# Kernel tuning notes

Hardware: AMD Instinct MI355X
Metric: run time of the kernel (lower is better)

The kernel has to match this reference:

```python
import jax, jax.numpy as jnp
import numpy as np

D_MODEL = 1024
N_HEADS = 16
D_HEAD = D_MODEL // N_HEADS


def setup_inputs() -> dict:
    key = jax.random.key(0)
    ks = jax.random.split(key, 11)
    B, S = 2, 2048
    scale = 1.0 / np.sqrt(D_MODEL)
    inp = {
        "query": jax.random.normal(ks[0], (B, S, D_MODEL), jnp.float32),
        "key": jax.random.normal(ks[1], (B, S, D_MODEL), jnp.float32),
        "value": jax.random.normal(ks[2], (B, S, D_MODEL), jnp.float32),
        "Wq": jax.random.normal(ks[3], (D_MODEL, D_MODEL), jnp.float32) * scale,
        "bq": jnp.zeros((D_MODEL,), jnp.float32),
        "Wk": jax.random.normal(ks[4], (D_MODEL, D_MODEL), jnp.float32) * scale,
        "bk": jnp.zeros((D_MODEL,), jnp.float32),
        "Wv": jax.random.normal(ks[5], (D_MODEL, D_MODEL), jnp.float32) * scale,
        "bv": jnp.zeros((D_MODEL,), jnp.float32),
        "Wo": jax.random.normal(ks[6], (D_MODEL, D_MODEL), jnp.float32) * scale,
        "bo": jnp.zeros((D_MODEL,), jnp.float32),
    }
    return inp


def _split_heads(x):
    B, S, _ = x.shape
    return x.reshape(B, S, N_HEADS, D_HEAD).transpose(0, 2, 1, 3)  # [B,H,S,Dh]


def reference(query, key, value, Wq, bq, Wk, bk, Wv, bv, Wo, bo):
    q = _split_heads(query @ Wq + bq)
    k = _split_heads(key @ Wk + bk)
    v = _split_heads(value @ Wv + bv)
    # scores [B,H,S,S] -- faithfully materialized as in the original
    scores = jnp.einsum("bhqd,bhkd->bhqk", q, k) / np.sqrt(D_HEAD)
    attn = jax.nn.softmax(scores, axis=-1)
    out = jnp.einsum("bhqk,bhkd->bhqd", attn, v)  # [B,H,S,Dh]
    B, H, S, Dh = out.shape
    out = out.transpose(0, 2, 1, 3).reshape(B, S, H * Dh)
    return out @ Wo + bo
```

## Files before the change

### kernel.cpp

```cpp
#include <hip/hip_runtime.h>
#include <hip/hip_bf16.h>

using bf16 = __hip_bfloat16;
typedef __bf16 bf16x8 __attribute__((ext_vector_type(8)));
typedef __bf16 bf16x2v __attribute__((ext_vector_type(2)));
typedef float f32x4 __attribute__((ext_vector_type(4)));
typedef float f32x16 __attribute__((ext_vector_type(16)));

#define SEQ 2048
#define DM  1024
#define QSCALE 0.18033688011112042f

__device__ __forceinline__ f32x4 mfma16(bf16x8 a, bf16x8 b, f32x4 c) {
  return __builtin_amdgcn_mfma_f32_16x16x32_bf16(a, b, c, 0, 0, 0);
}
__device__ __forceinline__ f32x16 mfma32(bf16x8 a, bf16x8 b, f32x16 c) {
  return __builtin_amdgcn_mfma_f32_32x32x16_bf16(a, b, c, 0, 0, 0);
}
__device__ __forceinline__ void gload16(const void* g, void* l) {
  __builtin_amdgcn_global_load_lds(
      (const __attribute__((address_space(1))) unsigned int*)g,
      (__attribute__((address_space(3))) unsigned int*)l, 16, 0, 0);
}
__device__ __forceinline__ unsigned short bfbits(float x) {
  bf16 h = __float2bfloat16(x);
  return *reinterpret_cast<unsigned short*>(&h);
}
__device__ __forceinline__ unsigned pk2(float a, float b) {
#if __has_builtin(__builtin_amdgcn_cvt_pk_bf16_f32)
  bf16x2v r = __builtin_amdgcn_cvt_pk_bf16_f32(a, b);
  return *reinterpret_cast<unsigned*>(&r);
#else
  return (unsigned)bfbits(a) | ((unsigned)bfbits(b) << 16);
#endif
}
__device__ __forceinline__ float fexp2(float x) {
#if __has_builtin(__builtin_amdgcn_exp2f)
  return __builtin_amdgcn_exp2f(x);
#else
  return exp2f(x);
#endif
}
__device__ __forceinline__ void plswap(unsigned& a, unsigned& b) {
  asm("v_permlane32_swap_b32 %0, %1" : "+v"(a), "+v"(b));
}

__global__ __launch_bounds__(256) void cast_all(const float* __restrict__ q,
                                                const float* __restrict__ k,
                                                const float* __restrict__ v,
                                                const float* __restrict__ Wq,
                                                const float* __restrict__ Wk,
                                                const float* __restrict__ Wv,
                                                const float* __restrict__ Wo,
                                                bf16* __restrict__ Lx,
                                                bf16* __restrict__ Lw,
                                                bf16* __restrict__ Lwo) {
  __shared__ float tf[64][68];
  if (blockIdx.y < 3) {
    const float* src = blockIdx.y == 0 ? q : (blockIdx.y == 1 ? k : v);
    bf16* dst = Lx + (size_t)blockIdx.y * (4096ull * 1024) + (size_t)blockIdx.x * 16384;
#pragma unroll
    for (int i = 0; i < 8; ++i) {
      int u = threadIdx.x + i * 256;
      int k32 = u >> 6, l = u & 63;
      const float* p = src + (size_t)(blockIdx.x * 16 + (l & 15)) * 1024 + k32 * 32 + (l >> 4) * 8;
      float4 a = *(const float4*)p;
      float4 b = *(const float4*)(p + 4);
      alignas(16) unsigned o[4] = {pk2(a.x, a.y), pk2(a.z, a.w), pk2(b.x, b.y), pk2(b.z, b.w)};
      *(uint4*)(dst + (size_t)u * 8) = *(const uint4*)o;
    }
    return;
  }
  const int widx = blockIdx.y - 3;
  const float* W = widx == 0 ? Wq : (widx == 1 ? Wk : (widx == 2 ? Wv : Wo));
  bf16* dst = widx < 3 ? (Lw + (size_t)widx * 1048576) : Lwo;
  const int t = threadIdx.x, bx = blockIdx.x & 15, by = blockIdx.x >> 4;
#pragma unroll
  for (int i = 0; i < 4; ++i) {
    int u = t + i * 256, r = u >> 4, c4 = u & 15;
    *(float4*)&tf[r][c4 * 4] = *(const float4*)(W + (size_t)(by * 64 + r) * 1024 + bx * 64 + c4 * 4);
  }
  __syncthreads();
#pragma unroll
  for (int i = 0; i < 2; ++i) {
    int u = t + i * 256;
    int sub = u >> 6, l = u & 63;
    int n16l = sub >> 1, k32l = sub & 1;
    int nn = n16l * 16 + (l & 15);
    int kk = k32l * 32 + (l >> 4) * 8;
    alignas(16) unsigned o[4];
#pragma unroll
    for (int p = 0; p < 4; ++p) o[p] = pk2(tf[kk + 2 * p][nn], tf[kk + 2 * p + 1][nn]);
    size_t off = ((((size_t)(bx * 4 + n16l)) * 32 + (by * 2 + k32l)) * 64 + l) * 8;
    *(uint4*)(dst + off) = *(const uint4*)o;
  }
}

__global__ __launch_bounds__(256) void qkv_gemm(const bf16* __restrict__ Lw,
                                                const bf16* __restrict__ Lx,
                                                const float* __restrict__ bq,
                                                const float* __restrict__ bk,
                                                const float* __restrict__ bv,
                                                bf16* __restrict__ Lq,
                                                bf16* __restrict__ Lk,
                                                bf16* __restrict__ Lv) {
  __shared__ alignas(16) bf16 Wl[8192];
  __shared__ alignas(16) bf16 Xl[8192];
  const int t = threadIdx.x, lane = t & 63, w = t >> 6;
  const int m16 = lane & 15, g4 = lane >> 4;
  const int third = blockIdx.y >> 3, mtl = blockIdx.y & 7, nt = blockIdx.x;
  const int wm = w >> 1, wn = w & 1;
  const bf16* Wb = Lw + (size_t)third * 1048576;
  const bf16* Xb = Lx + (size_t)third * (4096ull * 1024);
  f32x4 acc[4][4] = {};

  for (int slab = 0; slab < 16; ++slab) {
#pragma unroll
    for (int ii = 0; ii < 4; ++ii) {
      int s = w * 4 + ii;
      const bf16* gp = Wb + ((((size_t)(mtl * 8 + (s >> 1))) * 32 + slab * 2 + (s & 1)) * 64 + lane) * 8;
      gload16(gp, (void*)&Wl[s * 512]);
    }
#pragma unroll
    for (int ii = 0; ii < 4; ++ii) {
      int s = w * 4 + ii;
      const bf16* gp = Xb + ((((size_t)(nt * 8 + (s >> 1))) * 32 + slab * 2 + (s & 1)) * 64 + lane) * 8;
      gload16(gp, (void*)&Xl[s * 512]);
    }
    __syncthreads();
#pragma unroll
    for (int c = 0; c < 2; ++c) {
      bf16x8 wf[4], xf[4];
#pragma unroll
      for (int i = 0; i < 4; ++i) wf[i] = *(const bf16x8*)&Wl[((wm * 4 + i) * 2 + c) * 512 + lane * 8];
#pragma unroll
      for (int j = 0; j < 4; ++j) xf[j] = *(const bf16x8*)&Xl[((wn * 4 + j) * 2 + c) * 512 + lane * 8];
      if (third < 2) {
#pragma unroll
        for (int i = 0; i < 4; ++i)
#pragma unroll
          for (int j = 0; j < 4; ++j) acc[i][j] = mfma16(wf[i], xf[j], acc[i][j]);
      } else {
#pragma unroll
        for (int i = 0; i < 4; ++i)
#pragma unroll
          for (int j = 0; j < 4; ++j) acc[i][j] = mfma16(xf[i], wf[j], acc[i][j]);
      }
    }
    __syncthreads();
  }

  if (third < 2) {
    bf16* dst = third == 0 ? Lq : Lk;
    const float* bias = third == 0 ? bq : bk;
    const float sc = third == 0 ? QSCALE : 1.0f;
#pragma unroll
    for (int i = 0; i < 4; ++i) {
      int doutb = mtl * 128 + wm * 64 + i * 16 + g4 * 4;
      float4 b4 = *(const float4*)(bias + doutb);
      int hh = doutb >> 6, d32 = (doutb & 63) >> 5;
      int lhi = (doutb & 31) >> 3, half = g4 & 1;
#pragma unroll
      for (int j = 0; j < 4; ++j) {
        int seq = nt * 128 + wn * 64 + j * 16 + m16;
        int bb = seq >> 11, s16w = (seq & 2047) >> 4;
        size_t off = ((((size_t)(bb * 128 + s16w)) * 16 + hh) * 2 + d32) * 512 + (m16 + 16 * lhi) * 8 + half * 4;
        uint2 pv;
        pv.x = pk2((acc[i][j][0] + b4.x) * sc, (acc[i][j][1] + b4.y) * sc);
        pv.y = pk2((acc[i][j][2] + b4.z) * sc, (acc[i][j][3] + b4.w) * sc);
        *(uint2*)(dst + off) = pv;
      }
    }
  } else {
#pragma unroll
    for (int j = 0; j < 4; ++j) {
      int dout = mtl * 128 + wm * 64 + j * 16 + m16;
      float bvv = bv[dout];
      int hh = dout >> 6, dt = (dout & 63) >> 4;
#pragma unroll
      for (int i = 0; i < 4; ++i) {
        int seqb = nt * 128 + wn * 64 + i * 16 + g4 * 4;
        int bb = seqb >> 11, kt = (seqb & 2047) >> 6, ks32 = (seqb & 63) >> 5;
        int lhi = (seqb & 31) >> 3, half = g4 & 1;
        size_t off = (((((size_t)(bb * 32 + kt)) * 16 + hh) * 4 + dt) * 2 + ks32) * 512 + (m16 + 16 * lhi) * 8 + half * 4;
        uint2 pv;
        pv.x = pk2(acc[i][j][0] + bvv, acc[i][j][1] + bvv);
        pv.y = pk2(acc[i][j][2] + bvv, acc[i][j][3] + bvv);
        *(uint2*)(Lv + off) = pv;
      }
    }
  }
}

__global__ __launch_bounds__(512, 4) void flash(const bf16* __restrict__ Lq,
                                                const bf16* __restrict__ Lk,
                                                const bf16* __restrict__ Lv,
                                                bf16* __restrict__ Lab) {
  __shared__ alignas(16) unsigned char smem[65536];
  bf16* const Kb = (bf16*)smem;
  bf16* const Vb = (bf16*)(smem + 32768);

  const int t = threadIdx.x, lane = t & 63, w = t >> 6;
  const int l31 = lane & 31, m16 = lane & 15, hi = lane >> 5, b4 = (lane >> 4) & 1;
  const int qw = w >> 1, g = w & 1, wg = w >> 1;
  const int bid = blockIdx.x;
  const int logical = ((bid & 7) << 6) | (bid >> 3);
  const int qt = logical & 15, h = (logical >> 4) & 15, b = logical >> 8;

  bf16x8 qf[4];
  {
    const int sQ = b * 128 + qt * 8 + qw * 2 + b4;
#pragma unroll
    for (int ks = 0; ks < 4; ++ks) {
      const int d32 = ks >> 1, g4q = (ks & 1) * 2 + hi;
      qf[ks] = *(const bf16x8*)(Lq + (((size_t)sQ * 16 + h) * 2 + d32) * 512 + (m16 + 16 * g4q) * 8);
    }
  }

  const int ss = wg >> 1, sd = wg & 1;
#pragma unroll
  for (int u = 0; u < 2; ++u) {
    const bf16* gk = Lk + ((((size_t)(b * 128 + g * 64 + u * 2 + ss)) * 16 + h) * 2 + sd) * 512 + lane * 8;
    gload16(gk, (void*)(Kb + (g * 2 + 0) * 4096 + u * 2048 + wg * 512));
    const bf16* gv = Lv + (((((size_t)(b * 32 + g * 16)) * 16 + h) * 4 + wg) * 2 + u) * 512 + lane * 8;
    gload16(gv, (void*)(Vb + (g * 2 + 0) * 4096 + u * 2048 + wg * 512));
  }

  float lrow = 0.f;
  f32x16 oacc[2] = {};
  __syncthreads();

  for (int it = 0; it < 16; ++it) {
    const int cur = it & 1;
    const bf16* const Klb = Kb + (g * 2 + cur) * 4096;
    const bf16* const Vlb = Vb + (g * 2 + cur) * 4096;
    if (it < 15) {
      const int nb = cur ^ 1;
#pragma unroll
      for (int u = 0; u < 2; ++u) {
        const int kc = (it + 1) * 2 + u;
        const bf16* gk = Lk + ((((size_t)(b * 128 + g * 64 + kc * 2 + ss)) * 16 + h) * 2 + sd) * 512 + lane * 8;
        gload16(gk, (void*)(Kb + (g * 2 + nb) * 4096 + u * 2048 + wg * 512));
        const bf16* gv = Lv + (((((size_t)(b * 32 + g * 16 + (kc >> 1))) * 16 + h) * 4 + wg) * 2 + (kc & 1)) * 512 + lane * 8;
        gload16(gv, (void*)(Vb + (g * 2 + nb) * 4096 + u * 2048 + wg * 512));
      }
    }

#pragma unroll
    for (int u = 0; u < 2; ++u) {
      const bf16* const Kl = Klb + u * 2048;
      const bf16* const Vl = Vlb + u * 2048;

      f32x16 s = {};
      __builtin_amdgcn_s_setprio(1);
#pragma unroll
      for (int ks = 0; ks < 4; ++ks) {
        const int d32 = ks >> 1, g4k = (ks & 1) * 2 + hi;
        bf16x8 kf = *(const bf16x8*)&Kl[((b4 * 2 + d32) * 64 + m16 + 16 * g4k) * 8];
        s = mfma32(kf, qf[ks], s);
      }
      __builtin_amdgcn_s_setprio(0);

      float e[16];
#pragma unroll
      for (int r = 0; r < 16; ++r) e[r] = fexp2(s[r]);
      {
        float a0 = e[0] + e[1], a1 = e[2] + e[3], a2 = e[4] + e[5], a3 = e[6] + e[7];
        float a4 = e[8] + e[9], a5 = e[10] + e[11], a6 = e[12] + e[13], a7 = e[14] + e[15];
        lrow += ((a0 + a1) + (a2 + a3)) + ((a4 + a5) + (a6 + a7));
      }
      bf16x8 bP[2];
#pragma unroll
      for (int c = 0; c < 2; ++c) {
        unsigned P0 = pk2(e[8 * c + 0], e[8 * c + 1]);
        unsigned P1 = pk2(e[8 * c + 2], e[8 * c + 3]);
        unsigned P2 = pk2(e[8 * c + 4], e[8 * c + 5]);
        unsigned P3 = pk2(e[8 * c + 6], e[8 * c + 7]);
        plswap(P0, P2);
        plswap(P1, P3);
        alignas(16) unsigned pw[4] = {P0, P1, P2, P3};
        bP[c] = *(const bf16x8*)pw;
      }

      __builtin_amdgcn_s_setprio(1);
#pragma unroll
      for (int dtile = 0; dtile < 2; ++dtile) {
        const int dt = dtile * 2 + b4;
#pragma unroll
        for (int c = 0; c < 2; ++c) {
          bf16x8 av = *(const bf16x8*)&Vl[(dt * 64 + m16 + 16 * (2 * c + hi)) * 8];
          oacc[dtile] = mfma32(av, bP[c], oacc[dtile]);
        }
      }
      __builtin_amdgcn_s_setprio(0);
    }
    __syncthreads();
  }

  lrow += __shfl_xor(lrow, 32);

  float* const Os = (float*)smem;
  float* const Ls = (float*)(smem + 32768);
  if (g == 1) {
#pragma unroll
    for (int dtile = 0; dtile < 2; ++dtile)
#pragma unroll
      for (int r = 0; r < 16; ++r)
        Os[((qw * 2 + dtile) * 16 + r) * 64 + lane] = oacc[dtile][r];
    if (hi == 0) Ls[qw * 32 + l31] = lrow;
  }
  __syncthreads();
  if (g == 0) {
    const float inv = 1.f / (lrow + Ls[qw * 32 + l31]);
    const int sQ = b * 128 + qt * 8 + qw * 2 + b4;
#pragma unroll
    for (int dtile = 0; dtile < 2; ++dtile) {
      const int k32 = h * 2 + dtile;
#pragma unroll
      for (int j = 0; j < 8; ++j) {
        const int r = 2 * j;
        float o0 = oacc[dtile][r] + Os[((qw * 2 + dtile) * 16 + r) * 64 + lane];
        float o1 = oacc[dtile][r + 1] + Os[((qw * 2 + dtile) * 16 + r + 1) * 64 + lane];
        unsigned pv = pk2(o0 * inv, o1 * inv);
        size_t off = ((size_t)sQ * 32 + k32) * 512 + (m16 + 16 * (r >> 2)) * 8 + 4 * hi + (r & 3);
        *(unsigned*)(Lab + off) = pv;
      }
    }
  }
}

__global__ __launch_bounds__(256) void out_gemm(const bf16* __restrict__ Lab,
                                                const bf16* __restrict__ Lwo,
                                                const float* __restrict__ bo,
                                                float* __restrict__ out) {
  __shared__ alignas(16) bf16 Al[8192];
  __shared__ alignas(16) bf16 Bl[4096];
  const int t = threadIdx.x, lane = t & 63, w = t >> 6;
  const int m16 = lane & 15, g4 = lane >> 4;
  const int nt = blockIdx.x, mt = blockIdx.y;
  const int wm = w >> 1, wn = w & 1;
  f32x4 acc[4][2] = {};

  for (int slab = 0; slab < 16; ++slab) {
#pragma unroll
    for (int ii = 0; ii < 4; ++ii) {
      int s = w * 4 + ii;
      const bf16* gp = Lab + (((size_t)(mt * 8 + (s >> 1))) * 32 + slab * 2 + (s & 1)) * 512 + lane * 8;
      gload16(gp, (void*)&Al[s * 512]);
    }
#pragma unroll
    for (int ii = 0; ii < 2; ++ii) {
      int s = w * 2 + ii;
      const bf16* gp = Lwo + (((size_t)(nt * 4 + (s >> 1))) * 32 + slab * 2 + (s & 1)) * 512 + lane * 8;
      gload16(gp, (void*)&Bl[s * 512]);
    }
    __syncthreads();
#pragma unroll
    for (int c = 0; c < 2; ++c) {
      bf16x8 aA[4], bW[2];
#pragma unroll
      for (int i = 0; i < 4; ++i) aA[i] = *(const bf16x8*)&Al[((wm * 4 + i) * 2 + c) * 512 + lane * 8];
#pragma unroll
      for (int j = 0; j < 2; ++j) bW[j] = *(const bf16x8*)&Bl[((wn * 2 + j) * 2 + c) * 512 + lane * 8];
#pragma unroll
      for (int i = 0; i < 4; ++i)
#pragma unroll
        for (int j = 0; j < 2; ++j) acc[i][j] = mfma16(aA[i], bW[j], acc[i][j]);
    }
    __syncthreads();
  }
#pragma unroll
  for (int j = 0; j < 2; ++j) {
    int n = nt * 64 + wn * 32 + j * 16 + m16;
    float bb = bo[n];
#pragma unroll
    for (int i = 0; i < 4; ++i) {
      int seqb = mt * 128 + wm * 64 + i * 16 + g4 * 4;
#pragma unroll
      for (int r = 0; r < 4; ++r) out[(size_t)(seqb + r) * 1024 + n] = acc[i][j][r] + bb;
    }
  }
}

extern "C" void kernel_launch(void* const* d_in, const int* in_sizes, int n_in,
                              void* d_out, int out_size, void* d_ws, size_t ws_size,
                              hipStream_t stream) {
  const float* query = (const float*)d_in[0];
  const float* key   = (const float*)d_in[1];
  const float* value = (const float*)d_in[2];
  const float* Wq = (const float*)d_in[3];
  const float* bq = (const float*)d_in[4];
  const float* Wk = (const float*)d_in[5];
  const float* bk = (const float*)d_in[6];
  const float* Wv = (const float*)d_in[7];
  const float* bv = (const float*)d_in[8];
  const float* Wo = (const float*)d_in[9];
  const float* bo = (const float*)d_in[10];
  float* out = (float*)d_out;

  bf16* Lw  = (bf16*)d_ws;
  bf16* Lwo = Lw + 3ull * 1048576;
  bf16* Lx  = Lwo + 1048576;
  bf16* Lq  = Lx + 3ull * 4194304;
  bf16* Lk  = Lq + 4194304;
  bf16* Lv  = Lk + 4194304;
  bf16* Lab = Lv + 4194304;

  cast_all<<<dim3(256, 7), 256, 0, stream>>>(query, key, value, Wq, Wk, Wv, Wo, Lx, Lw, Lwo);
  qkv_gemm<<<dim3(32, 24), 256, 0, stream>>>(Lw, Lx, bq, bk, bv, Lq, Lk, Lv);
  flash<<<512, 512, 0, stream>>>(Lq, Lk, Lv, Lab);
  out_gemm<<<dim3(16, 32), 256, 0, stream>>>(Lab, Lwo, bo, out);
}
```

Baseline: 215.2 us.

## Double-buffer QKV GEMM with larger 256x256 tiles and XCD-aware block remap

The QKV projection GEMM moves from 128x128 tiles with 256 threads to 256x256 tiles with 512 threads. Shared-memory loads are double-buffered so the next K slab is fetched while MFMAs run on the current one, and one barrier per slab replaces two. Block indices are remapped so neighbouring logical tiles land on the same XCD, and s_setprio raises wave priority around the MFMA bursts. In exchange the grid drops to 192 blocks on a 256-CU device, and each thread holds more accumulator registers and more LDS.

Measured after the change: 215.1 us. No clear change (-0.0%).

```diff
diff --git a/kernel.cpp b/kernel.cpp
--- a/kernel.cpp
+++ b/kernel.cpp
@@ -96,58 +96,76 @@
   }
 }
 
-__global__ __launch_bounds__(256) void qkv_gemm(const bf16* __restrict__ Lw,
-                                                const bf16* __restrict__ Lx,
-                                                const float* __restrict__ bq,
-                                                const float* __restrict__ bk,
-                                                const float* __restrict__ bv,
-                                                bf16* __restrict__ Lq,
-                                                bf16* __restrict__ Lk,
-                                                bf16* __restrict__ Lv) {
-  __shared__ alignas(16) bf16 Wl[8192];
-  __shared__ alignas(16) bf16 Xl[8192];
+__global__ __launch_bounds__(512, 2) void qkv_gemm(const bf16* __restrict__ Lw,
+                                                   const bf16* __restrict__ Lx,
+                                                   const float* __restrict__ bq,
+                                                   const float* __restrict__ bk,
+                                                   const float* __restrict__ bv,
+                                                   bf16* __restrict__ Lq,
+                                                   bf16* __restrict__ Lk,
+                                                   bf16* __restrict__ Lv) {
+  __shared__ alignas(16) bf16 At[2][16384];
+  __shared__ alignas(16) bf16 Bt[2][16384];
   const int t = threadIdx.x, lane = t & 63, w = t >> 6;
   const int m16 = lane & 15, g4 = lane >> 4;
-  const int third = blockIdx.y >> 3, mtl = blockIdx.y & 7, nt = blockIdx.x;
-  const int wm = w >> 1, wn = w & 1;
+  const int bid = blockIdx.y * 16 + blockIdx.x;
+  const int logical = (bid & 7) * 24 + (bid >> 3);
+  const int nt = logical & 15, ym = logical >> 4;
+  const int third = ym >> 2, mt = ym & 3;
+  const int wm = w >> 2, wn = w & 3;
   const bf16* Wb = Lw + (size_t)third * 1048576;
   const bf16* Xb = Lx + (size_t)third * (4096ull * 1024);
-  f32x4 acc[4][4] = {};
-
+  f32x4 acc[8][4] = {};
+
+#pragma unroll
+  for (int ii = 0; ii < 4; ++ii) {
+    int u = w * 4 + ii;
+    gload16(Wb + (((size_t)(mt * 16 + (u >> 1)) * 32 + (u & 1)) * 64 + lane) * 8, (void*)&At[0][u * 512]);
+    gload16(Xb + (((size_t)(nt * 16 + (u >> 1)) * 32 + (u & 1)) * 64 + lane) * 8, (void*)&Bt[0][u * 512]);
+  }
+  __syncthreads();
+
+  const bf16* Ab0 = (third < 2) ? At[0] : Bt[0];
+  const bf16* Bb0 = (third < 2) ? Bt[0] : At[0];
+
+  int cur = 0;
   for (int slab = 0; slab < 16; ++slab) {
-#pragma unroll
-    for (int ii = 0; ii < 4; ++ii) {
-      int s = w * 4 + ii;
-      const bf16* gp = Wb + ((((size_t)(mtl * 8 + (s >> 1))) * 32 + slab * 2 + (s & 1)) * 64 + lane) * 8;
-      gload16(gp, (void*)&Wl[s * 512]);
-    }
-#pragma unroll
-    for (int ii = 0; ii < 4; ++ii) {
-      int s = w * 4 + ii;
-      const bf16* gp = Xb + ((((size_t)(nt * 8 + (s >> 1))) * 32 + slab * 2 + (s & 1)) * 64 + lane) * 8;
-      gload16(gp, (void*)&Xl[s * 512]);
+    if (slab < 15) {
+      const int nb = cur ^ 1, k2 = (slab + 1) * 2;
+#pragma unroll
+      for (int ii = 0; ii < 4; ++ii) {
+        int u = w * 4 + ii;
+        gload16(Wb + (((size_t)(mt * 16 + (u >> 1)) * 32 + k2 + (u & 1)) * 64 + lane) * 8,
+                (void*)&At[nb][u * 512]);
+        gload16(Xb + (((size_t)(nt * 16 + (u >> 1)) * 32 + k2 + (u & 1)) * 64 + lane) * 8,
+                (void*)&Bt[nb][u * 512]);
+      }
+    }
+    const bf16* Ac = Ab0 + cur * 16384;
+    const bf16* Bc = Bb0 + cur * 16384;
+#pragma unroll
+    for (int kc = 0; kc < 2; ++kc) {
+      bf16x8 bfr[4];
+#pragma unroll
+      for (int nj = 0; nj < 4; ++nj)
+        bfr[nj] = *(const bf16x8*)&Bc[((wn * 4 + nj) * 2 + kc) * 512 + lane * 8];
+#pragma unroll
+      for (int mh = 0; mh < 2; ++mh) {
+        bf16x8 afr[4];
+#pragma unroll
+        for (int i = 0; i < 4; ++i)
+          afr[i] = *(const bf16x8*)&Ac[((wm * 8 + mh * 4 + i) * 2 + kc) * 512 + lane * 8];
+        __builtin_amdgcn_s_setprio(1);
+#pragma unroll
+        for (int i = 0; i < 4; ++i)
+#pragma unroll
+          for (int nj = 0; nj < 4; ++nj)
+            acc[mh * 4 + i][nj] = mfma16(afr[i], bfr[nj], acc[mh * 4 + i][nj]);
+        __builtin_amdgcn_s_setprio(0);
+      }
     }
     __syncthreads();
-#pragma unroll
-    for (int c = 0; c < 2; ++c) {
-      bf16x8 wf[4], xf[4];
-#pragma unroll
-      for (int i = 0; i < 4; ++i) wf[i] = *(const bf16x8*)&Wl[((wm * 4 + i) * 2 + c) * 512 + lane * 8];
-#pragma unroll
-      for (int j = 0; j < 4; ++j) xf[j] = *(const bf16x8*)&Xl[((wn * 4 + j) * 2 + c) * 512 + lane * 8];
-      if (third < 2) {
-#pragma unroll
-        for (int i = 0; i < 4; ++i)
-#pragma unroll
-          for (int j = 0; j < 4; ++j) acc[i][j] = mfma16(wf[i], xf[j], acc[i][j]);
-      } else {
-#pragma unroll
-        for (int i = 0; i < 4; ++i)
-#pragma unroll
-          for (int j = 0; j < 4; ++j) acc[i][j] = mfma16(xf[i], wf[j], acc[i][j]);
-      }
-    }
-    __syncthreads();
+    cur ^= 1;
   }
 
   if (third < 2) {
@@ -155,37 +173,37 @@
     const float* bias = third == 0 ? bq : bk;
     const float sc = third == 0 ? QSCALE : 1.0f;
 #pragma unroll
-    for (int i = 0; i < 4; ++i) {
-      int doutb = mtl * 128 + wm * 64 + i * 16 + g4 * 4;
+    for (int mi = 0; mi < 8; ++mi) {
+      int doutb = mt * 256 + wm * 128 + mi * 16 + g4 * 4;
       float4 b4 = *(const float4*)(bias + doutb);
       int hh = doutb >> 6, d32 = (doutb & 63) >> 5;
       int lhi = (doutb & 31) >> 3, half = g4 & 1;
 #pragma unroll
-      for (int j = 0; j < 4; ++j) {
-        int seq = nt * 128 + wn * 64 + j * 16 + m16;
-        int bb = seq >> 11, s16w = (seq & 2047) >> 4;
-        size_t off = ((((size_t)(bb * 128 + s16w)) * 16 + hh) * 2 + d32) * 512 + (m16 + 16 * lhi) * 8 + half * 4;
+      for (int nj = 0; nj < 4; ++nj) {
+        int seq = nt * 256 + wn * 64 + nj * 16 + m16;
+        int bb2 = seq >> 11, s16w = (seq & 2047) >> 4;
+        size_t off = ((((size_t)(bb2 * 128 + s16w)) * 16 + hh) * 2 + d32) * 512 + (m16 + 16 * lhi) * 8 + half * 4;
         uint2 pv;
-        pv.x = pk2((acc[i][j][0] + b4.x) * sc, (acc[i][j][1] + b4.y) * sc);
-        pv.y = pk2((acc[i][j][2] + b4.z) * sc, (acc[i][j][3] + b4.w) * sc);
+        pv.x = pk2((acc[mi][nj][0] + b4.x) * sc, (acc[mi][nj][1] + b4.y) * sc);
+        pv.y = pk2((acc[mi][nj][2] + b4.z) * sc, (acc[mi][nj][3] + b4.w) * sc);
         *(uint2*)(dst + off) = pv;
       }
     }
   } else {
 #pragma unroll
-    for (int j = 0; j < 4; ++j) {
-      int dout = mtl * 128 + wm * 64 + j * 16 + m16;
+    for (int nj = 0; nj < 4; ++nj) {
+      int dout = mt * 256 + wn * 64 + nj * 16 + m16;
       float bvv = bv[dout];
       int hh = dout >> 6, dt = (dout & 63) >> 4;
 #pragma unroll
-      for (int i = 0; i < 4; ++i) {
-        int seqb = nt * 128 + wn * 64 + i * 16 + g4 * 4;
-        int bb = seqb >> 11, kt = (seqb & 2047) >> 6, ks32 = (seqb & 63) >> 5;
+      for (int mi = 0; mi < 8; ++mi) {
+        int seqb = nt * 256 + wm * 128 + mi * 16 + g4 * 4;
+        int b_ = seqb >> 11, kt = (seqb & 2047) >> 6, ks32 = (seqb & 63) >> 5;
         int lhi = (seqb & 31) >> 3, half = g4 & 1;
-        size_t off = (((((size_t)(bb * 32 + kt)) * 16 + hh) * 4 + dt) * 2 + ks32) * 512 + (m16 + 16 * lhi) * 8 + half * 4;
+        size_t off = (((((size_t)(b_ * 32 + kt)) * 16 + hh) * 4 + dt) * 2 + ks32) * 512 + (m16 + 16 * lhi) * 8 + half * 4;
         uint2 pv;
-        pv.x = pk2(acc[i][j][0] + bvv, acc[i][j][1] + bvv);
-        pv.y = pk2(acc[i][j][2] + bvv, acc[i][j][3] + bvv);
+        pv.x = pk2(acc[mi][nj][0] + bvv, acc[mi][nj][1] + bvv);
+        pv.y = pk2(acc[mi][nj][2] + bvv, acc[mi][nj][3] + bvv);
         *(uint2*)(Lv + off) = pv;
       }
     }
@@ -407,7 +425,7 @@
   bf16* Lab = Lv + 4194304;
 
   cast_all<<<dim3(256, 7), 256, 0, stream>>>(query, key, value, Wq, Wk, Wv, Wo, Lx, Lw, Lwo);
-  qkv_gemm<<<dim3(32, 24), 256, 0, stream>>>(Lw, Lx, bq, bk, bv, Lq, Lk, Lv);
+  qkv_gemm<<<dim3(16, 12), 512, 0, stream>>>(Lw, Lx, bq, bk, bv, Lq, Lk, Lv);
   flash<<<512, 512, 0, stream>>>(Lq, Lk, Lv, Lab);
   out_gemm<<<dim3(16, 32), 256, 0, stream>>>(Lab, Lwo, bo, out);
 }
```
